# Kernel tuning notes

Hardware: AMD Instinct MI355X
Metric: run time of the kernel (lower is better)

Reference implementation:

```python
import jax, jax.numpy as jnp
import numpy as np
from jax import lax

NUM_CLASSES = 7
NUM_ANCHORS = 5
IGNORE_THRES = 0.6
EPS = 1e-12

ANCHORS = np.array([[1.08, 1.19], [3.42, 4.41], [6.63, 11.38], [9.42, 5.11], [16.62, 10.52]], dtype=np.float32)


def setup_inputs():
    key = jax.random.key(0)
    k1, k2, k3, k4, k5, k6 = jax.random.split(key, 6)
    nB, nT = 16, 50
    nH = nW = 152
    nCh = NUM_ANCHORS * (7 + NUM_CLASSES)
    x = jax.random.normal(k6, (nB, nCh, nH, nW), dtype=jnp.float32)
    labels = jax.random.randint(k1, (nB, nT), 0, NUM_CLASSES).astype(jnp.float32)
    cxy = jax.random.uniform(k2, (nB, nT, 2), minval=0.02, maxval=0.98)
    wl = jax.random.uniform(k3, (nB, nT, 2), minval=0.02, maxval=0.2)
    imre = jax.random.uniform(k4, (nB, nT, 2), minval=-1.0, maxval=1.0)
    target = jnp.concatenate([labels[..., None], cxy, wl, imre], axis=-1)
    nvalid = jax.random.randint(k5, (nB,), 10, nT + 1)
    tmask = (jnp.arange(nT)[None, :] < nvalid[:, None]).astype(jnp.float32)
    target = target * tmask[..., None]  # zero-pad trailing boxes
    anchors = jnp.asarray(ANCHORS)
    return {"x": x, "target": target, "anchors": anchors}


def iou_center(b1, b2):
    # marvis pytorch-yolo2 bbox_ious, center (cx,cy,w,h) format, no +1
    mx = jnp.minimum(b1[..., 0] - b1[..., 2] / 2, b2[..., 0] - b2[..., 2] / 2)
    Mx = jnp.maximum(b1[..., 0] + b1[..., 2] / 2, b2[..., 0] + b2[..., 2] / 2)
    my = jnp.minimum(b1[..., 1] - b1[..., 3] / 2, b2[..., 1] - b2[..., 3] / 2)
    My = jnp.maximum(b1[..., 1] + b1[..., 3] / 2, b2[..., 1] + b2[..., 3] / 2)
    cw = b1[..., 2] + b2[..., 2] - (Mx - mx)
    ch = b1[..., 3] + b2[..., 3] - (My - my)
    carea = jnp.where((cw <= 0) | (ch <= 0), 0.0, cw * ch)
    uarea = b1[..., 2] * b1[..., 3] + b2[..., 2] * b2[..., 3] - carea
    return carea / uarea


def build_targets(pred_boxes, target, anchors, nH, nW):
    nB, nT, _ = target.shape
    nA = anchors.shape[0]
    nC = NUM_CLASSES
    dtype = pred_boxes.dtype
    scale = jnp.array([nW, nH, nW, nH], dtype=dtype)
    g = target[:, :, 1:5] * scale  # [nB,nT,4] = (gx,gy,gw,gl) in grid units
    # loop-1 breaks at first box with x==0 -> prefix validity
    valid_prefix = jnp.cumprod((target[:, :, 1] != 0).astype(jnp.int32), axis=1).astype(bool)
    # loop-2 skips rows whose full sum is 0
    valid = jnp.sum(target, axis=2) != 0

    # ignore mask: max IoU of every predicted box vs every (prefix-)valid gt
    def step(cur, inp):
        gt, v = inp  # gt [nB,4], v [nB]
        iou = iou_center(pred_boxes, gt[:, None, None, None, :])  # [nB,nA,nH,nW]
        return jnp.maximum(cur, jnp.where(v[:, None, None, None], iou, 0.0)), None

    cur_ious, _ = lax.scan(step, jnp.zeros(pred_boxes.shape[:4], dtype),
                           (jnp.moveaxis(g, 1, 0), jnp.moveaxis(valid_prefix, 1, 0)))
    conf_mask = (cur_ious <= IGNORE_THRES).astype(dtype)

    gx, gy, gw, gl = g[..., 0], g[..., 1], g[..., 2], g[..., 3]
    gi = jnp.clip(gx.astype(jnp.int32), 0, nW - 1)
    gj = jnp.clip(gy.astype(jnp.int32), 0, nH - 1)
    aw, ah = anchors[:, 0], anchors[:, 1]
    # eriklindernoren bbox_iou default x1y1x2y2=True on (0,0,w,l) boxes (+1 convention)
    inter = (jnp.clip(jnp.minimum(gw[..., None], aw) + 1.0, 0.0)
             * jnp.clip(jnp.minimum(gl[..., None], ah) + 1.0, 0.0))
    a_gt = (gw + 1.0) * (gl + 1.0)
    a_an = (aw + 1.0) * (ah + 1.0)
    anch_ious = inter / (a_gt[..., None] + a_an - inter + 1e-16)  # [nB,nT,nA]
    best_n = jnp.argmax(anch_ious, axis=-1)  # [nB,nT]

    b_idx = jnp.broadcast_to(jnp.arange(nB)[:, None], (nB, nT))
    N = nB * nA * nH * nW
    flat_idx = jnp.where(valid, ((b_idx * nA + best_n) * nH + gj) * nW + gi, -1)  # [nB,nT]
    fi = flat_idx.reshape(-1)

    # conf_mask zeroing for anchors whose shape-IoU exceeds ignore_thres at (gj,gi)
    a_ar = jnp.arange(nA)
    idx0 = ((b_idx[..., None] * nA + a_ar) * nH + gj[..., None]) * nW + gi[..., None]
    idx0 = jnp.where(valid[..., None] & (anch_ious > IGNORE_THRES), idx0, -1).reshape(-1)
    conf_flat = conf_mask.reshape(-1).at[idx0].set(0.0, mode='drop')
    conf_flat = conf_flat.at[fi].set(1.0, mode='drop')
    conf_mask = conf_flat.reshape(nB, nA, nH, nW)

    def scat(vals):
        return jnp.zeros((N,), dtype).at[fi].set(vals.reshape(-1), mode='drop').reshape(nB, nA, nH, nW)

    mask = scat(jnp.ones_like(gx))
    tx = scat(gx - gi.astype(dtype))
    ty = scat(gy - gj.astype(dtype))
    tw = scat(jnp.log(gw / aw[best_n] + 1e-16))
    tl = scat(jnp.log(gl / ah[best_n] + 1e-16))
    tim = scat(target[..., 5])
    tre = scat(target[..., 6])
    tconf = mask
    label = target[..., 0].astype(jnp.int32)
    onehot = jax.nn.one_hot(label, nC, dtype=dtype).reshape(-1, nC)
    tcls = jnp.zeros((N, nC), dtype).at[fi].set(onehot, mode='drop').reshape(nB, nA, nH, nW, nC)
    return mask, conf_mask, tx, ty, tw, tl, tconf, tcls, tim, tre


def _forward(x, target, anchors):
    nB, _, nH, nW = x.shape
    nA, nC = NUM_ANCHORS, NUM_CLASSES
    pred = x.reshape(nB, nA, 7 + nC, nH, nW).transpose(0, 1, 3, 4, 2)  # [nB,nA,nH,nW,7+nC]
    px = jax.nn.sigmoid(pred[..., 0])
    py = jax.nn.sigmoid(pred[..., 1])
    pw = pred[..., 2]
    pl = pred[..., 3]
    pim = pred[..., 4]
    pre = pred[..., 5]
    pconf = jax.nn.sigmoid(pred[..., 6])
    pcls = jax.nn.softmax(pred[..., 7:], axis=-1)

    grid_x = jnp.arange(nW, dtype=x.dtype).reshape(1, 1, 1, nW)
    grid_y = jnp.arange(nH, dtype=x.dtype).reshape(1, 1, nH, 1)
    aw = anchors[:, 0].reshape(1, nA, 1, 1)
    ah = anchors[:, 1].reshape(1, nA, 1, 1)
    pred_boxes = jnp.stack([px + grid_x, py + grid_y,
                            jnp.exp(pw) * aw, jnp.exp(pl) * ah], axis=-1)
    # build_targets consumes detached data in the original (.data / .cpu())
    pred_boxes = lax.stop_gradient(pred_boxes)
    tgt = lax.stop_gradient(target)
    anc = lax.stop_gradient(anchors)
    mask, conf_mask, tx, ty, tw, tl, tconf, tcls, tim, tre = build_targets(pred_boxes, tgt, anc, nH, nW)

    m = mask
    nM = jnp.maximum(jnp.sum(m), 1.0)

    def mmse(a, t):  # nn.MSELoss mean over masked elements
        return jnp.sum(((a - t) ** 2) * m) / nM

    loss_x = mmse(px, tx)
    loss_y = mmse(py, ty)
    loss_w = mmse(pw, tw)
    loss_h = mmse(pl, tl)
    loss_euler = mmse(pim, tim) + mmse(pre, tre)

    cf = conf_mask * (1.0 - m)  # conf_mask - mask
    ct = m
    p = jnp.clip(pconf, EPS, 1.0 - EPS)
    bce = -(tconf * jnp.log(p) + (1.0 - tconf) * jnp.log(1.0 - p))
    loss_conf = (jnp.sum(bce * cf) / jnp.maximum(jnp.sum(cf), 1.0)
                 + jnp.sum(bce * ct) / jnp.maximum(jnp.sum(ct), 1.0))

    # original applies CrossEntropyLoss (log_softmax) on already-softmaxed probs
    logp = jax.nn.log_softmax(pcls, axis=-1)
    ce = -jnp.sum(tcls * logp, axis=-1)
    loss_cls = (1.0 / nB) * jnp.sum(ce * m) / nM

    return loss_x + loss_y + loss_w + loss_h + loss_conf + loss_cls + loss_euler


def reference(x, target, anchors):
    return _forward(x, target, anchors)
```

## Files before the change

### kernel.cpp

```cpp
#include <hip/hip_runtime.h>

#define NB 16
#define NT 50
#define NA 5
#define NH 152
#define NW 152
#define CH 70
#define HW (NH*NW)
#define AHW (NA*HW)
#define NCELL (NB*AHW)
#define NTGT (NB*NT)

#define NSUMB 452
#define SUM_IT 4
#define GRID_FUSED (NSUMB + NTGT + 1)
#define CAP 2944

#define S_SUM 0
#define S_SUB 452
#define S_CNT (S_SUB + 801)
#define S_WIN (S_CNT + 801)

__device__ __forceinline__ float sp_f(float v) {
    return (v > 20.f) ? v : __logf(1.f + __expf(v));
}

struct Box { float xlo, xhi, ylo, yhi, w, h, qb; };

__device__ __forceinline__ Box build_box(const float* __restrict__ xp,
                                         float aw, float ah, int i, int j) {
    #pragma clang fp contract(off)
    float l0 = xp[0], l1 = xp[HW], l2 = xp[2 * HW], l3 = xp[3 * HW];
    float sx = 1.f / (1.f + __expf(-l0));
    float sy = 1.f / (1.f + __expf(-l1));
    float bxv = (float)i + sx;
    float byv = (float)j + sy;
    float bw = __expf(l2) * aw, bh = __expf(l3) * ah;
    float hw2 = 0.5f * bw, hh2 = 0.5f * bh;
    Box o;
    o.xlo = bxv - hw2; o.xhi = bxv + hw2;
    o.ylo = byv - hh2; o.yhi = byv + hh2;
    o.w = bw; o.h = bh; o.qb = 0.375f * bw * bh;
    return o;
}

__device__ __forceinline__ bool excl_eval(const Box& bb, int i, int j, int a,
                                          int valid, int validp,
                                          int gi, int gj, int bn, int am,
                                          float xlo, float xhi, float ylo, float yhi,
                                          float gw, float gl, float q) {
    #pragma clang fp contract(off)
    if (valid && i == gi && j == gj && (a == bn || ((am >> a) & 1))) return true;
    if (validp) {
        float mx = fminf(bb.xlo, xlo), Mx = fmaxf(bb.xhi, xhi);
        float my = fminf(bb.ylo, ylo), My = fmaxf(bb.yhi, yhi);
        float cw = bb.w + gw - (Mx - mx);
        float ch = bb.h + gl - (My - my);
        if (cw > 0.f && ch > 0.f && cw * ch > bb.qb + q) return true;
    }
    return false;
}

__device__ __forceinline__ void win_terms(const float* __restrict__ xp,
                                          float tx, float ty, float twv, float tlv,
                                          float timv, float trev, int lab,
                                          float* __restrict__ o) {
    float l[14];
    #pragma unroll
    for (int c = 0; c < 14; ++c) l[c] = xp[c * HW];
    float px = 1.f / (1.f + __expf(-l[0]));
    float py = 1.f / (1.f + __expf(-l[1]));
    o[0] = (px - tx) * (px - tx);
    o[1] = (py - ty) * (py - ty);
    float dw = l[2] - twv; o[2] = dw * dw;
    float dh = l[3] - tlv; o[3] = dh * dh;
    float di = l[4] - timv, dr = l[5] - trev;
    o[4] = di * di + dr * dr;
    o[5] = sp_f(-l[6]);
    float mx = l[7];
    #pragma unroll
    for (int c = 8; c < 14; ++c) mx = fmaxf(mx, l[c]);
    float e[7], se = 0.f;
    #pragma unroll
    for (int c = 0; c < 7; ++c) { e[c] = __expf(l[7 + c] - mx); se += e[c]; }
    float se2 = 0.f, slab = 0.f;
    #pragma unroll
    for (int c = 0; c < 7; ++c) {
        float s = e[c] / se;
        se2 += __expf(s);
        if (c == lab) slab = s;
    }
    o[6] = __logf(se2) - slab;
    o[7] = 1.f;
}

__global__ void __launch_bounds__(256) k_fused(const float* __restrict__ x,
                                               const float* __restrict__ tgt,
                                               const float* __restrict__ anc,
                                               float* __restrict__ ws) {
    __shared__ float redA[256], redB[256];
    int tid = threadIdx.x, bx = blockIdx.x;

    if (bx < NSUMB) {
        float s = 0.f;
        for (int it = 0; it < SUM_IT; ++it) {
            int c4 = (((it * NSUMB + bx) * 256) + tid) * 4;
            if (c4 < NCELL) {
                int b = c4 / AHW;
                int within = c4 - b * AHW;
                int a = within / HW;
                int rem = within - a * HW;
                const float* p = x + (size_t)(b * CH + a * 14 + 6) * HW + rem;
                float4 v = *(const float4*)p;
                s += sp_f(v.x) + sp_f(v.y) + sp_f(v.z) + sp_f(v.w);
            }
        }
        redA[tid] = s;
        __syncthreads();
        for (int st = 128; st > 0; st >>= 1) {
            if (tid < st) redA[tid] += redA[tid + st];
            __syncthreads();
        }
        if (tid == 0) ws[S_SUM + bx] = redA[0];
        return;
    }

    __shared__ float s_gx[NT + 1], s_gy[NT + 1], s_gw[NT + 1], s_gl[NT + 1];
    __shared__ float s_xlo[NT + 1], s_xhi[NT + 1], s_ylo[NT + 1], s_yhi[NT + 1];
    __shared__ float s_q[NT + 1], s_tim[NT], s_tre[NT], s_tw[NT], s_tl[NT];
    __shared__ int s_nz[NT], s_valid[NT + 1], s_validp[NT + 1];
    __shared__ int s_gi[NT + 1], s_gj[NT + 1], s_bn[NT + 1], s_am[NT + 1], s_lab[NT];
    __shared__ float s_aw[NA], s_ah[NA];
    __shared__ int s_stack[CAP];
    __shared__ int s_n, s_wrap, s_dup;

    int w = bx - NSUMB;
    bool isC = (w == NTGT);
    int b = isC ? (NB - 1) : (w / NT);
    int t = isC ? NT : (w - b * NT);

    if (tid < NA) { s_aw[tid] = anc[2 * tid]; s_ah[tid] = anc[2 * tid + 1]; }
    if (tid == 0) { s_n = 0; s_wrap = 0; s_dup = 0; }
    if (tid < NT) {
        const float* tp = tgt + (size_t)(b * NT + tid) * 7;
        float lab = tp[0], cx = tp[1], cy = tp[2], w7 = tp[3], l7 = tp[4];
        float ti = tp[5], tr = tp[6];
        s_nz[tid] = (cx != 0.f) ? 1 : 0;
        s_valid[tid] = ((lab + cx + cy + w7 + l7 + ti + tr) != 0.f) ? 1 : 0;
        float gx = cx * NW, gy = cy * NH, gw = w7 * NW, gl = l7 * NH;
        s_gx[tid] = gx; s_gy[tid] = gy; s_gw[tid] = gw; s_gl[tid] = gl;
        s_xlo[tid] = gx - 0.5f * gw; s_xhi[tid] = gx + 0.5f * gw;
        s_ylo[tid] = gy - 0.5f * gl; s_yhi[tid] = gy + 0.5f * gl;
        s_q[tid] = 0.375f * gw * gl;
        s_gi[tid] = min(max((int)gx, 0), NW - 1);
        s_gj[tid] = min(max((int)gy, 0), NH - 1);
        float agt = (gw + 1.f) * (gl + 1.f);
        float best = -1.f; int bn = 0, am = 0;
        float awb = 1.f, ahb = 1.f;
        for (int a = 0; a < NA; ++a) {
            float aw = anc[2 * a], ah = anc[2 * a + 1];
            float iw = fmaxf(fminf(gw, aw) + 1.f, 0.f);
            float ih = fmaxf(fminf(gl, ah) + 1.f, 0.f);
            float inter = iw * ih;
            float aan = (aw + 1.f) * (ah + 1.f);
            float iou = inter / (agt + aan - inter + 1e-16f);
            if (iou > best) { best = iou; bn = a; awb = aw; ahb = ah; }
            if (iou > 0.6f) am |= (1 << a);
        }
        s_bn[tid] = bn; s_am[tid] = am;
        s_tw[tid] = logf(gw / awb + 1e-16f);
        s_tl[tid] = logf(gl / ahb + 1e-16f);
        s_tim[tid] = ti; s_tre[tid] = tr;
        s_lab[tid] = ((int)lab) & 7;
    }
    __syncthreads();

    if (tid < NT) {
        int vp = 1;
        for (int u = 0; u <= tid; ++u) vp &= s_nz[u];
        s_validp[tid] = vp;
    }
    if (isC) {
        for (int id = tid; id < NTGT; id += 256) {
            const float* tp = tgt + (size_t)id * 7;
            float s7 = tp[0] + tp[1] + tp[2] + tp[3] + tp[4] + tp[5] + tp[6];
            if (s7 == 0.f) s_wrap = 1;
        }
    } else if (s_valid[t]) {
        int t2 = t + 1 + tid;
        if (t2 < NT && s_valid[t2] &&
            s_gi[t2] == s_gi[t] && s_gj[t2] == s_gj[t] && s_bn[t2] == s_bn[t])
            s_dup = 1;
    }
    __syncthreads();

    if (tid == 0) {
        s_valid[NT] = isC ? s_wrap : 0;
        s_validp[NT] = 0;
        s_gi[NT] = NW - 1; s_gj[NT] = NH - 1; s_bn[NT] = NA - 1; s_am[NT] = 0;
        s_gx[NT] = 0.f; s_gy[NT] = 0.f; s_gw[NT] = 0.f; s_gl[NT] = 0.f;
        s_xlo[NT] = 0.f; s_xhi[NT] = 0.f; s_ylo[NT] = 0.f; s_yhi[NT] = 0.f;
        s_q[NT] = 0.f;
    }
    __syncthreads();

    if (tid == 0) {
        float slot[8] = {0.f, 0.f, 0.f, 0.f, 0.f, 0.f, 0.f, 0.f};
        if (isC) {
            if (s_wrap) {
                const float* xp = x + (size_t)((NB - 1) * CH + (NA - 1) * 14) * HW
                                  + (HW - 1);
                float L16 = logf(1e-16f);
                win_terms(xp, 0.f, 0.f, L16, L16, 0.f, 0.f, 0, slot);
            }
        } else if (s_valid[t] && !s_dup) {
            const float* xp = x + (size_t)(b * CH + s_bn[t] * 14) * HW
                              + s_gj[t] * NW + s_gi[t];
            win_terms(xp, s_gx[t] - (float)s_gi[t], s_gy[t] - (float)s_gj[t],
                      s_tw[t], s_tl[t], s_tim[t], s_tre[t], s_lab[t], slot);
        }
        float* dst = ws + S_WIN + w * 8;
        #pragma unroll
        for (int k = 0; k < 8; ++k) dst[k] = slot[k];
    }

    bool vp = s_validp[t] && s_gw[t] > 0.f && s_gl[t] > 0.f;
    int i_lo = 0, j_lo = 0, W = 0, Hh = 0, rectTotal = 0;
    if (vp) {
        float gw3 = s_gw[t] * (1.f / 3.f), gl3 = s_gl[t] * (1.f / 3.f);
        i_lo = max(0, (int)floorf(s_gx[t] - gw3) - 1);
        int i_hi = min(NW - 1, (int)floorf(s_gx[t] + gw3) + 1);
        j_lo = max(0, (int)floorf(s_gy[t] - gl3) - 1);
        int j_hi = min(NH - 1, (int)floorf(s_gy[t] + gl3) + 1);
        W = i_hi - i_lo + 1; Hh = j_hi - j_lo + 1;
        rectTotal = W * Hh * NA;
    }
    int extra = (s_valid[t] && !vp) ? NA : 0;
    int total = rectTotal + extra;
    for (int idx = tid; idx < total; idx += 256) {
        int i, j, a;
        if (idx < rectTotal) {
            int dx = idx % W;
            int q2 = idx / W;
            j = j_lo + q2 % Hh;
            a = q2 / Hh;
            i = i_lo + dx;
        } else {
            a = idx - rectTotal; i = s_gi[t]; j = s_gj[t];
            if (!(a == s_bn[t] || ((s_am[t] >> a) & 1))) continue;
        }
        const float* xp = x + (size_t)(b * CH + a * 14) * HW + j * NW + i;
        Box bb = build_box(xp, s_aw[a], s_ah[a], i, j);
        if (excl_eval(bb, i, j, a, s_valid[t], s_validp[t],
                      s_gi[t], s_gj[t], s_bn[t], s_am[t],
                      s_xlo[t], s_xhi[t], s_ylo[t], s_yhi[t],
                      s_gw[t], s_gl[t], s_q[t])) {
            int pos = atomicAdd(&s_n, 1);
            if (pos < CAP) s_stack[pos] = (a << 16) | (j << 8) | i;
        }
    }
    __syncthreads();

    int n = min(s_n, CAP);
    float sub = 0.f, cnt = 0.f;
    for (int k = tid; k < n; k += 256) {
        int pk = s_stack[k];
        int i = pk & 255, j = (pk >> 8) & 255, a = pk >> 16;
        const float* xp = x + (size_t)(b * CH + a * 14) * HW + j * NW + i;
        Box bb = build_box(xp, s_aw[a], s_ah[a], i, j);
        bool owned = true;
        for (int u = 0; u < t; ++u) {
            if (excl_eval(bb, i, j, a, s_valid[u], s_validp[u],
                          s_gi[u], s_gj[u], s_bn[u], s_am[u],
                          s_xlo[u], s_xhi[u], s_ylo[u], s_yhi[u],
                          s_gw[u], s_gl[u], s_q[u])) { owned = false; break; }
        }
        if (owned) {
            sub += sp_f(xp[6 * HW]);
            cnt += 1.f;
        }
    }
    redA[tid] = sub; redB[tid] = cnt;
    __syncthreads();
    for (int st = 128; st > 0; st >>= 1) {
        if (tid < st) { redA[tid] += redA[tid + st]; redB[tid] += redB[tid + st]; }
        __syncthreads();
    }
    if (tid == 0) { ws[S_SUB + w] = redA[0]; ws[S_CNT + w] = redB[0]; }
}

__global__ void __launch_bounds__(256) k_reduce2(const float* __restrict__ ws,
                                                 float* __restrict__ out) {
    int tid = threadIdx.x;
    double acc[11];
    #pragma unroll
    for (int k = 0; k < 11; ++k) acc[k] = 0.0;
    for (int s = tid; s < NTGT + 1; s += 256) {
        const float* p = ws + S_WIN + s * 8;
        #pragma unroll
        for (int k = 0; k < 8; ++k) acc[k] += (double)p[k];
        acc[8] += (double)ws[S_SUB + s];
        acc[9] += (double)ws[S_CNT + s];
    }
    for (int s = tid; s < NSUMB; s += 256) acc[10] += (double)ws[S_SUM + s];

    __shared__ double R[11][256];
    #pragma unroll
    for (int k = 0; k < 11; ++k) R[k][tid] = acc[k];
    __syncthreads();
    for (int st = 128; st > 0; st >>= 1) {
        if (tid < st) {
            #pragma unroll
            for (int k = 0; k < 11; ++k) R[k][tid] += R[k][tid + st];
        }
        __syncthreads();
    }
    if (tid == 0) {
        double nM  = fmax(R[7][0], 1.0);
        double scf = fmax((double)NCELL - R[9][0], 1.0);
        double bce = R[10][0] - R[8][0];
        double loss =
            (R[0][0] + R[1][0] + R[2][0] + R[3][0] + R[4][0] + R[5][0]) / nM
            + bce / scf
            + (1.0 / NB) * R[6][0] / nM;
        out[0] = (float)loss;
    }
}

extern "C" void kernel_launch(void* const* d_in, const int* in_sizes, int n_in,
                              void* d_out, int out_size, void* d_ws, size_t ws_size,
                              hipStream_t stream) {
    const float* x   = (const float*)d_in[0];
    const float* tgt = (const float*)d_in[1];
    const float* anc = (const float*)d_in[2];
    float* ws  = (float*)d_ws;
    float* out = (float*)d_out;

    hipLaunchKernelGGL(k_fused, dim3(GRID_FUSED), dim3(256), 0, stream,
                       x, tgt, anc, ws);
    hipLaunchKernelGGL(k_reduce2, dim3(1), dim3(256), 0, stream, ws, out);
}
```

Measured before the change: 32.97 us.

## Split each target's ignore-rectangle work across four blocks by row bands

Each target's candidate rectangle is now divided into four row bands, each handled by its own block, so the grid grows from one block per target to four. Only the first band block computes the duplicate check and the window loss terms. This is meant to shorten the critical path of blocks with large rectangles and to shrink the shared stack so occupancy can rise. In exchange, every block redundantly recomputes the per-image target preprocessing, and the final reduction reads more partial sums.

```diff
diff --git a/kernel.cpp b/kernel.cpp
--- a/kernel.cpp
+++ b/kernel.cpp
@@ -10,16 +10,18 @@
 #define AHW (NA*HW)
 #define NCELL (NB*AHW)
 #define NTGT (NB*NT)
+#define SPLIT 4
 
 #define NSUMB 452
 #define SUM_IT 4
-#define GRID_FUSED (NSUMB + NTGT + 1)
-#define CAP 2944
+#define NRECT (NTGT*SPLIT)
+#define GRID_FUSED (NSUMB + NRECT + 1)
+#define CAP 768
 
 #define S_SUM 0
 #define S_SUB 452
-#define S_CNT (S_SUB + 801)
-#define S_WIN (S_CNT + 801)
+#define S_CNT (S_SUB + NRECT + 1)
+#define S_WIN (S_CNT + NRECT + 1)
 
 __device__ __forceinline__ float sp_f(float v) {
     return (v > 20.f) ? v : __logf(1.f + __expf(v));
@@ -135,9 +137,11 @@
     __shared__ int s_n, s_wrap, s_dup;
 
     int w = bx - NSUMB;
-    bool isC = (w == NTGT);
-    int b = isC ? (NB - 1) : (w / NT);
-    int t = isC ? NT : (w - b * NT);
+    bool isC = (w == NRECT);
+    int tt  = isC ? NTGT : (w / SPLIT);
+    int sub = isC ? 0 : (w % SPLIT);
+    int b = isC ? (NB - 1) : (tt / NT);
+    int t = isC ? NT : (tt - b * NT);
 
     if (tid < NA) { s_aw[tid] = anc[2 * tid]; s_ah[tid] = anc[2 * tid + 1]; }
     if (tid == 0) { s_n = 0; s_wrap = 0; s_dup = 0; }
@@ -176,9 +180,9 @@
     __syncthreads();
 
     if (tid < NT) {
-        int vp = 1;
-        for (int u = 0; u <= tid; ++u) vp &= s_nz[u];
-        s_validp[tid] = vp;
+        int vp2 = 1;
+        for (int u = 0; u <= tid; ++u) vp2 &= s_nz[u];
+        s_validp[tid] = vp2;
     }
     if (isC) {
         for (int id = tid; id < NTGT; id += 256) {
@@ -186,7 +190,7 @@
             float s7 = tp[0] + tp[1] + tp[2] + tp[3] + tp[4] + tp[5] + tp[6];
             if (s7 == 0.f) s_wrap = 1;
         }
-    } else if (s_valid[t]) {
+    } else if (sub == 0 && s_valid[t]) {
         int t2 = t + 1 + tid;
         if (t2 < NT && s_valid[t2] &&
             s_gi[t2] == s_gi[t] && s_gj[t2] == s_gj[t] && s_bn[t2] == s_bn[t])
@@ -204,7 +208,7 @@
     }
     __syncthreads();
 
-    if (tid == 0) {
+    if (tid == 0 && sub == 0) {
         float slot[8] = {0.f, 0.f, 0.f, 0.f, 0.f, 0.f, 0.f, 0.f};
         if (isC) {
             if (s_wrap) {
@@ -219,31 +223,35 @@
             win_terms(xp, s_gx[t] - (float)s_gi[t], s_gy[t] - (float)s_gj[t],
                       s_tw[t], s_tl[t], s_tim[t], s_tre[t], s_lab[t], slot);
         }
-        float* dst = ws + S_WIN + w * 8;
+        float* dst = ws + S_WIN + tt * 8;
         #pragma unroll
         for (int k = 0; k < 8; ++k) dst[k] = slot[k];
     }
 
     bool vp = s_validp[t] && s_gw[t] > 0.f && s_gl[t] > 0.f;
-    int i_lo = 0, j_lo = 0, W = 0, Hh = 0, rectTotal = 0;
+    int i_lo = 0, jb = 0, W = 0, rows = 0, rectTotal = 0;
     if (vp) {
         float gw3 = s_gw[t] * (1.f / 3.f), gl3 = s_gl[t] * (1.f / 3.f);
         i_lo = max(0, (int)floorf(s_gx[t] - gw3) - 1);
         int i_hi = min(NW - 1, (int)floorf(s_gx[t] + gw3) + 1);
-        j_lo = max(0, (int)floorf(s_gy[t] - gl3) - 1);
+        int j_lo = max(0, (int)floorf(s_gy[t] - gl3) - 1);
         int j_hi = min(NH - 1, (int)floorf(s_gy[t] + gl3) + 1);
-        W = i_hi - i_lo + 1; Hh = j_hi - j_lo + 1;
-        rectTotal = W * Hh * NA;
-    }
-    int extra = (s_valid[t] && !vp) ? NA : 0;
+        W = i_hi - i_lo + 1;
+        int Hh = j_hi - j_lo + 1;
+        jb = j_lo + (Hh * sub) / SPLIT;
+        int je = j_lo + (Hh * (sub + 1)) / SPLIT;
+        rows = je - jb;
+        rectTotal = W * rows * NA;
+    }
+    int extra = (s_valid[t] && !vp && sub == 0) ? NA : 0;
     int total = rectTotal + extra;
     for (int idx = tid; idx < total; idx += 256) {
         int i, j, a;
         if (idx < rectTotal) {
             int dx = idx % W;
             int q2 = idx / W;
-            j = j_lo + q2 % Hh;
-            a = q2 / Hh;
+            j = jb + q2 % rows;
+            a = q2 / rows;
             i = i_lo + dx;
         } else {
             a = idx - rectTotal; i = s_gi[t]; j = s_gj[t];
@@ -262,7 +270,7 @@
     __syncthreads();
 
     int n = min(s_n, CAP);
-    float sub = 0.f, cnt = 0.f;
+    float sub_s = 0.f, cnt_s = 0.f;
     for (int k = tid; k < n; k += 256) {
         int pk = s_stack[k];
         int i = pk & 255, j = (pk >> 8) & 255, a = pk >> 16;
@@ -276,11 +284,11 @@
                           s_gw[u], s_gl[u], s_q[u])) { owned = false; break; }
         }
         if (owned) {
-            sub += sp_f(xp[6 * HW]);
-            cnt += 1.f;
-        }
-    }
-    redA[tid] = sub; redB[tid] = cnt;
+            sub_s += sp_f(xp[6 * HW]);
+            cnt_s += 1.f;
+        }
+    }
+    redA[tid] = sub_s; redB[tid] = cnt_s;
     __syncthreads();
     for (int st = 128; st > 0; st >>= 1) {
         if (tid < st) { redA[tid] += redA[tid + st]; redB[tid] += redB[tid + st]; }
@@ -299,6 +307,8 @@
         const float* p = ws + S_WIN + s * 8;
         #pragma unroll
         for (int k = 0; k < 8; ++k) acc[k] += (double)p[k];
+    }
+    for (int s = tid; s < NRECT + 1; s += 256) {
         acc[8] += (double)ws[S_SUB + s];
         acc[9] += (double)ws[S_CNT + s];
     }
```

Result: slower. 38.91 us (+18.0%).

## Split per-batch target preprocessing into a separate prep kernel

Applied to the files above, without the earlier changes.

Moves the per-target preprocessing (grid coords, anchor matching, prefix validity, duplicate detection, wrap flag) out of each of the 801 target blocks into a 16-block prep kernel that writes packed metadata to the workspace. The main kernel then only loads precomputed values, and the target blocks come first in the grid with the softplus-sum blocks after them. This removes redundant per-block work (every block used to recompute all 50 targets of its batch) but adds an extra kernel launch and a global-memory round trip.

```diff
diff --git a/kernel.cpp b/kernel.cpp
--- a/kernel.cpp
+++ b/kernel.cpp
@@ -13,13 +13,28 @@
 
 #define NSUMB 452
 #define SUM_IT 4
-#define GRID_FUSED (NSUMB + NTGT + 1)
+#define GRID_MAIN (NTGT + 1 + NSUMB)
 #define CAP 2944
 
-#define S_SUM 0
-#define S_SUB 452
-#define S_CNT (S_SUB + 801)
-#define S_WIN (S_CNT + 801)
+#define P_GX   0
+#define P_GY   800
+#define P_GW   1600
+#define P_GL   2400
+#define P_XLO  3200
+#define P_XHI  4000
+#define P_YLO  4800
+#define P_YHI  5600
+#define P_Q    6400
+#define P_TW   7200
+#define P_TL   8000
+#define P_TIM  8800
+#define P_TRE  9600
+#define P_META 10400
+#define S_SUM  11264
+#define S_SUB  11716
+#define S_CNT  12517
+#define S_WIN  13318
+
 
 __device__ __forceinline__ float sp_f(float v) {
     return (v > 20.f) ? v : __logf(1.f + __expf(v));
@@ -94,68 +109,28 @@
     o[7] = 1.f;
 }
 
-__global__ void __launch_bounds__(256) k_fused(const float* __restrict__ x,
-                                               const float* __restrict__ tgt,
-                                               const float* __restrict__ anc,
-                                               float* __restrict__ ws) {
-    __shared__ float redA[256], redB[256];
-    int tid = threadIdx.x, bx = blockIdx.x;
-
-    if (bx < NSUMB) {
-        float s = 0.f;
-        for (int it = 0; it < SUM_IT; ++it) {
-            int c4 = (((it * NSUMB + bx) * 256) + tid) * 4;
-            if (c4 < NCELL) {
-                int b = c4 / AHW;
-                int within = c4 - b * AHW;
-                int a = within / HW;
-                int rem = within - a * HW;
-                const float* p = x + (size_t)(b * CH + a * 14 + 6) * HW + rem;
-                float4 v = *(const float4*)p;
-                s += sp_f(v.x) + sp_f(v.y) + sp_f(v.z) + sp_f(v.w);
-            }
-        }
-        redA[tid] = s;
-        __syncthreads();
-        for (int st = 128; st > 0; st >>= 1) {
-            if (tid < st) redA[tid] += redA[tid + st];
-            __syncthreads();
-        }
-        if (tid == 0) ws[S_SUM + bx] = redA[0];
-        return;
-    }
-
-    __shared__ float s_gx[NT + 1], s_gy[NT + 1], s_gw[NT + 1], s_gl[NT + 1];
-    __shared__ float s_xlo[NT + 1], s_xhi[NT + 1], s_ylo[NT + 1], s_yhi[NT + 1];
-    __shared__ float s_q[NT + 1], s_tim[NT], s_tre[NT], s_tw[NT], s_tl[NT];
-    __shared__ int s_nz[NT], s_valid[NT + 1], s_validp[NT + 1];
-    __shared__ int s_gi[NT + 1], s_gj[NT + 1], s_bn[NT + 1], s_am[NT + 1], s_lab[NT];
-    __shared__ float s_aw[NA], s_ah[NA];
-    __shared__ int s_stack[CAP];
-    __shared__ int s_n, s_wrap, s_dup;
-
-    int w = bx - NSUMB;
-    bool isC = (w == NTGT);
-    int b = isC ? (NB - 1) : (w / NT);
-    int t = isC ? NT : (w - b * NT);
-
-    if (tid < NA) { s_aw[tid] = anc[2 * tid]; s_ah[tid] = anc[2 * tid + 1]; }
-    if (tid == 0) { s_n = 0; s_wrap = 0; s_dup = 0; }
+__global__ void __launch_bounds__(256) k_prep(const float* __restrict__ tgt,
+                                              const float* __restrict__ anc,
+                                              float* __restrict__ ws) {
+    __shared__ int s_nz[NT], s_valid[NT], s_gi[NT], s_gj[NT], s_bn[NT];
+    __shared__ int s_wrap;
+    int tid = threadIdx.x, b = blockIdx.x;
+    if (tid == 0) s_wrap = 0;
+
+    float gx = 0.f, gy = 0.f, gw = 0.f, gl = 0.f, ti = 0.f, tr = 0.f;
+    float twv = 0.f, tlv = 0.f;
+    int bn = 0, am = 0, lab = 0;
     if (tid < NT) {
         const float* tp = tgt + (size_t)(b * NT + tid) * 7;
-        float lab = tp[0], cx = tp[1], cy = tp[2], w7 = tp[3], l7 = tp[4];
-        float ti = tp[5], tr = tp[6];
+        float l7 = tp[0], cx = tp[1], cy = tp[2], w7 = tp[3], h7 = tp[4];
+        ti = tp[5]; tr = tp[6];
         s_nz[tid] = (cx != 0.f) ? 1 : 0;
-        s_valid[tid] = ((lab + cx + cy + w7 + l7 + ti + tr) != 0.f) ? 1 : 0;
-        float gx = cx * NW, gy = cy * NH, gw = w7 * NW, gl = l7 * NH;
-        s_gx[tid] = gx; s_gy[tid] = gy; s_gw[tid] = gw; s_gl[tid] = gl;
-        s_xlo[tid] = gx - 0.5f * gw; s_xhi[tid] = gx + 0.5f * gw;
-        s_ylo[tid] = gy - 0.5f * gl; s_yhi[tid] = gy + 0.5f * gl;
-        s_q[tid] = 0.375f * gw * gl;
+        s_valid[tid] = ((l7 + cx + cy + w7 + h7 + ti + tr) != 0.f) ? 1 : 0;
+        gx = cx * NW; gy = cy * NH; gw = w7 * NW; gl = h7 * NH;
         s_gi[tid] = min(max((int)gx, 0), NW - 1);
         s_gj[tid] = min(max((int)gy, 0), NH - 1);
         float agt = (gw + 1.f) * (gl + 1.f);
-        float best = -1.f; int bn = 0, am = 0;
+        float best = -1.f;
         float awb = 1.f, ahb = 1.f;
         for (int a = 0; a < NA; ++a) {
             float aw = anc[2 * a], ah = anc[2 * a + 1];
@@ -167,64 +142,155 @@
             if (iou > best) { best = iou; bn = a; awb = aw; ahb = ah; }
             if (iou > 0.6f) am |= (1 << a);
         }
-        s_bn[tid] = bn; s_am[tid] = am;
-        s_tw[tid] = logf(gw / awb + 1e-16f);
-        s_tl[tid] = logf(gl / ahb + 1e-16f);
-        s_tim[tid] = ti; s_tre[tid] = tr;
-        s_lab[tid] = ((int)lab) & 7;
-    }
-    __syncthreads();
-
-    if (tid < NT) {
-        int vp = 1;
-        for (int u = 0; u <= tid; ++u) vp &= s_nz[u];
-        s_validp[tid] = vp;
-    }
-    if (isC) {
+        s_bn[tid] = bn;
+        twv = logf(gw / awb + 1e-16f);
+        tlv = logf(gl / ahb + 1e-16f);
+        lab = ((int)l7) & 7;
+    }
+    if (b == 0) {
         for (int id = tid; id < NTGT; id += 256) {
             const float* tp = tgt + (size_t)id * 7;
             float s7 = tp[0] + tp[1] + tp[2] + tp[3] + tp[4] + tp[5] + tp[6];
             if (s7 == 0.f) s_wrap = 1;
         }
-    } else if (s_valid[t]) {
-        int t2 = t + 1 + tid;
-        if (t2 < NT && s_valid[t2] &&
-            s_gi[t2] == s_gi[t] && s_gj[t2] == s_gj[t] && s_bn[t2] == s_bn[t])
-            s_dup = 1;
     }
     __syncthreads();
 
-    if (tid == 0) {
-        s_valid[NT] = isC ? s_wrap : 0;
-        s_validp[NT] = 0;
-        s_gi[NT] = NW - 1; s_gj[NT] = NH - 1; s_bn[NT] = NA - 1; s_am[NT] = 0;
-        s_gx[NT] = 0.f; s_gy[NT] = 0.f; s_gw[NT] = 0.f; s_gl[NT] = 0.f;
-        s_xlo[NT] = 0.f; s_xhi[NT] = 0.f; s_ylo[NT] = 0.f; s_yhi[NT] = 0.f;
-        s_q[NT] = 0.f;
+    if (tid < NT) {
+        int id = b * NT + tid;
+        int vp = 1;
+        for (int u = 0; u <= tid; ++u) vp &= s_nz[u];
+        int dup = 0;
+        if (s_valid[tid]) {
+            for (int t2 = tid + 1; t2 < NT; ++t2) {
+                if (s_valid[t2] && s_gi[t2] == s_gi[tid] &&
+                    s_gj[t2] == s_gj[tid] && s_bn[t2] == s_bn[tid]) { dup = 1; break; }
+            }
+        }
+        ws[P_GX + id]  = gx;  ws[P_GY + id]  = gy;
+        ws[P_GW + id]  = gw;  ws[P_GL + id]  = gl;
+        ws[P_XLO + id] = gx - 0.5f * gw; ws[P_XHI + id] = gx + 0.5f * gw;
+        ws[P_YLO + id] = gy - 0.5f * gl; ws[P_YHI + id] = gy + 0.5f * gl;
+        ws[P_Q + id]   = 0.375f * gw * gl;
+        ws[P_TW + id]  = twv; ws[P_TL + id] = tlv;
+        ws[P_TIM + id] = ti;  ws[P_TRE + id] = tr;
+        ((int*)ws)[P_META + id] =
+            s_gi[tid] | (s_gj[tid] << 8) | (s_bn[tid] << 16) | (am << 19)
+            | (s_valid[tid] << 24) | (vp << 25) | (dup << 26) | (lab << 27);
+    }
+    if (b == 0 && tid == 0) ((int*)ws)[P_META + NTGT] = s_wrap;
+}
+
+__global__ void __launch_bounds__(256) k_main(const float* __restrict__ x,
+                                              const float* __restrict__ anc,
+                                              float* __restrict__ ws) {
+    __shared__ float redA[256], redB[256];
+    int tid = threadIdx.x, bx = blockIdx.x;
+
+    if (bx > NTGT) {
+        int sx = bx - NTGT - 1;
+        float s = 0.f;
+        for (int it = 0; it < SUM_IT; ++it) {
+            int c4 = (((it * NSUMB + sx) * 256) + tid) * 4;
+            if (c4 < NCELL) {
+                int b = c4 / AHW;
+                int within = c4 - b * AHW;
+                int a = within / HW;
+                int rem = within - a * HW;
+                const float* p = x + (size_t)(b * CH + a * 14 + 6) * HW + rem;
+                float4 v = *(const float4*)p;
+                s += sp_f(v.x) + sp_f(v.y) + sp_f(v.z) + sp_f(v.w);
+            }
+        }
+        redA[tid] = s;
+        __syncthreads();
+        for (int st = 128; st > 0; st >>= 1) {
+            if (tid < st) redA[tid] += redA[tid + st];
+            __syncthreads();
+        }
+        if (tid == 0) ws[S_SUM + sx] = redA[0];
+        return;
+    }
+
+    __shared__ float s_gx[NT], s_gy[NT], s_gw[NT], s_gl[NT];
+    __shared__ float s_xlo[NT], s_xhi[NT], s_ylo[NT], s_yhi[NT], s_q[NT];
+    __shared__ int s_meta[NT];
+    __shared__ float s_aw[NA], s_ah[NA];
+    __shared__ int s_stack[CAP];
+    __shared__ int s_n;
+
+    bool isC = (bx == NTGT);
+    int tt = isC ? (NTGT - 1) : bx;
+    int b = tt / NT;
+    int t = isC ? NT : (tt - b * NT);
+
+    if (tid < NA) { s_aw[tid] = anc[2 * tid]; s_ah[tid] = anc[2 * tid + 1]; }
+    if (tid == 0) s_n = 0;
+    if (tid < NT) {
+        int id = b * NT + tid;
+        s_gx[tid] = ws[P_GX + id];  s_gy[tid] = ws[P_GY + id];
+        s_gw[tid] = ws[P_GW + id];  s_gl[tid] = ws[P_GL + id];
+        s_xlo[tid] = ws[P_XLO + id]; s_xhi[tid] = ws[P_XHI + id];
+        s_ylo[tid] = ws[P_YLO + id]; s_yhi[tid] = ws[P_YHI + id];
+        s_q[tid] = ws[P_Q + id];
+        s_meta[tid] = ((const int*)ws)[P_META + id];
     }
     __syncthreads();
 
-    if (tid == 0) {
-        float slot[8] = {0.f, 0.f, 0.f, 0.f, 0.f, 0.f, 0.f, 0.f};
-        if (isC) {
-            if (s_wrap) {
+    auto excl_u = [&](const Box& bb, int i, int j, int a, int u) -> bool {
+        int m = s_meta[u];
+        return excl_eval(bb, i, j, a, (m >> 24) & 1, (m >> 25) & 1,
+                         m & 255, (m >> 8) & 255, (m >> 16) & 7, (m >> 19) & 31,
+                         s_xlo[u], s_xhi[u], s_ylo[u], s_yhi[u],
+                         s_gw[u], s_gl[u], s_q[u]);
+    };
+
+    if (isC) {
+        if (tid == 0) {
+            int wrap = ((const int*)ws)[P_META + NTGT];
+            float slot[8] = {0.f, 0.f, 0.f, 0.f, 0.f, 0.f, 0.f, 0.f};
+            float sub = 0.f, cnt = 0.f;
+            if (wrap) {
                 const float* xp = x + (size_t)((NB - 1) * CH + (NA - 1) * 14) * HW
                                   + (HW - 1);
                 float L16 = logf(1e-16f);
                 win_terms(xp, 0.f, 0.f, L16, L16, 0.f, 0.f, 0, slot);
+                int i = NW - 1, j = NH - 1, a = NA - 1;
+                Box bb = build_box(xp, s_aw[a], s_ah[a], i, j);
+                bool any = false;
+                for (int u = 0; u < NT; ++u)
+                    if (excl_u(bb, i, j, a, u)) { any = true; break; }
+                if (!any) { sub = sp_f(xp[6 * HW]); cnt = 1.f; }
             }
-        } else if (s_valid[t] && !s_dup) {
-            const float* xp = x + (size_t)(b * CH + s_bn[t] * 14) * HW
-                              + s_gj[t] * NW + s_gi[t];
-            win_terms(xp, s_gx[t] - (float)s_gi[t], s_gy[t] - (float)s_gj[t],
-                      s_tw[t], s_tl[t], s_tim[t], s_tre[t], s_lab[t], slot);
-        }
-        float* dst = ws + S_WIN + w * 8;
+            float* dst = ws + S_WIN + NTGT * 8;
+            #pragma unroll
+            for (int k = 0; k < 8; ++k) dst[k] = slot[k];
+            ws[S_SUB + NTGT] = sub;
+            ws[S_CNT + NTGT] = cnt;
+        }
+        return;
+    }
+
+    int mt = s_meta[t];
+    int valid = (mt >> 24) & 1, validp = (mt >> 25) & 1, dup = (mt >> 26) & 1;
+    int gi = mt & 255, gj = (mt >> 8) & 255, bn = (mt >> 16) & 7;
+    int am = (mt >> 19) & 31, lab = (mt >> 27) & 7;
+
+    if (tid == 0) {
+        float slot[8] = {0.f, 0.f, 0.f, 0.f, 0.f, 0.f, 0.f, 0.f};
+        if (valid && !dup) {
+            int id = tt;
+            const float* xp = x + (size_t)(b * CH + bn * 14) * HW + gj * NW + gi;
+            win_terms(xp, s_gx[t] - (float)gi, s_gy[t] - (float)gj,
+                      ws[P_TW + id], ws[P_TL + id],
+                      ws[P_TIM + id], ws[P_TRE + id], lab, slot);
+        }
+        float* dst = ws + S_WIN + tt * 8;
         #pragma unroll
         for (int k = 0; k < 8; ++k) dst[k] = slot[k];
     }
 
-    bool vp = s_validp[t] && s_gw[t] > 0.f && s_gl[t] > 0.f;
+    bool vp = validp && s_gw[t] > 0.f && s_gl[t] > 0.f;
     int i_lo = 0, j_lo = 0, W = 0, Hh = 0, rectTotal = 0;
     if (vp) {
         float gw3 = s_gw[t] * (1.f / 3.f), gl3 = s_gl[t] * (1.f / 3.f);
@@ -235,7 +301,7 @@
         W = i_hi - i_lo + 1; Hh = j_hi - j_lo + 1;
         rectTotal = W * Hh * NA;
     }
-    int extra = (s_valid[t] && !vp) ? NA : 0;
+    int extra = (valid && !vp) ? NA : 0;
     int total = rectTotal + extra;
     for (int idx = tid; idx < total; idx += 256) {
         int i, j, a;
@@ -246,15 +312,12 @@
             a = q2 / Hh;
             i = i_lo + dx;
         } else {
-            a = idx - rectTotal; i = s_gi[t]; j = s_gj[t];
-            if (!(a == s_bn[t] || ((s_am[t] >> a) & 1))) continue;
+            a = idx - rectTotal; i = gi; j = gj;
+            if (!(a == bn || ((am >> a) & 1))) continue;
         }
         const float* xp = x + (size_t)(b * CH + a * 14) * HW + j * NW + i;
         Box bb = build_box(xp, s_aw[a], s_ah[a], i, j);
-        if (excl_eval(bb, i, j, a, s_valid[t], s_validp[t],
-                      s_gi[t], s_gj[t], s_bn[t], s_am[t],
-                      s_xlo[t], s_xhi[t], s_ylo[t], s_yhi[t],
-                      s_gw[t], s_gl[t], s_q[t])) {
+        if (excl_u(bb, i, j, a, t)) {
             int pos = atomicAdd(&s_n, 1);
             if (pos < CAP) s_stack[pos] = (a << 16) | (j << 8) | i;
         }
@@ -262,31 +325,27 @@
     __syncthreads();
 
     int n = min(s_n, CAP);
-    float sub = 0.f, cnt = 0.f;
+    float sub_s = 0.f, cnt_s = 0.f;
     for (int k = tid; k < n; k += 256) {
         int pk = s_stack[k];
         int i = pk & 255, j = (pk >> 8) & 255, a = pk >> 16;
         const float* xp = x + (size_t)(b * CH + a * 14) * HW + j * NW + i;
         Box bb = build_box(xp, s_aw[a], s_ah[a], i, j);
         bool owned = true;
-        for (int u = 0; u < t; ++u) {
-            if (excl_eval(bb, i, j, a, s_valid[u], s_validp[u],
-                          s_gi[u], s_gj[u], s_bn[u], s_am[u],
-                          s_xlo[u], s_xhi[u], s_ylo[u], s_yhi[u],
-                          s_gw[u], s_gl[u], s_q[u])) { owned = false; break; }
-        }
+        for (int u = 0; u < t; ++u)
+            if (excl_u(bb, i, j, a, u)) { owned = false; break; }
         if (owned) {
-            sub += sp_f(xp[6 * HW]);
-            cnt += 1.f;
-        }
-    }
-    redA[tid] = sub; redB[tid] = cnt;
+            sub_s += sp_f(xp[6 * HW]);
+            cnt_s += 1.f;
+        }
+    }
+    redA[tid] = sub_s; redB[tid] = cnt_s;
     __syncthreads();
     for (int st = 128; st > 0; st >>= 1) {
         if (tid < st) { redA[tid] += redA[tid + st]; redB[tid] += redB[tid + st]; }
         __syncthreads();
     }
-    if (tid == 0) { ws[S_SUB + w] = redA[0]; ws[S_CNT + w] = redB[0]; }
+    if (tid == 0) { ws[S_SUB + tt] = redA[0]; ws[S_CNT + tt] = redB[0]; }
 }
 
 __global__ void __launch_bounds__(256) k_reduce2(const float* __restrict__ ws,
@@ -336,7 +395,7 @@
     float* ws  = (float*)d_ws;
     float* out = (float*)d_out;
 
-    hipLaunchKernelGGL(k_fused, dim3(GRID_FUSED), dim3(256), 0, stream,
-                       x, tgt, anc, ws);
+    hipLaunchKernelGGL(k_prep, dim3(NB), dim3(256), 0, stream, tgt, anc, ws);
+    hipLaunchKernelGGL(k_main, dim3(GRID_MAIN), dim3(256), 0, stream, x, anc, ws);
     hipLaunchKernelGGL(k_reduce2, dim3(1), dim3(256), 0, stream, ws, out);
 }
```

Measured after the change: 41.91 us. +27.1%, slower.
